# Optimization experiments

Measured on AMD Instinct MI355X. Metric: run time of the kernel, lower is better.

Reference implementation:

```python
import jax, jax.numpy as jnp
import numpy as np

B, F, C, H, W = 16, 256, 64, 64, 64   # batch, features, z_channels(e_dim), height, width
N_E = 512                              # codebooksize
BETA = 1.0
EPS = 1e-5


def setup_inputs() -> dict:
    key = jax.random.key(0)
    ks = jax.random.split(key, 4)
    x = jax.random.normal(ks[0], (B, F, H, W), jnp.float32)
    emb = jax.random.normal(ks[1], (N_E, C), jnp.float32)
    emb = emb / jnp.linalg.norm(emb, axis=1, keepdims=True)  # points on hypersphere
    return dict(
        x=x,
        bn1_gamma=jnp.ones((F,), jnp.float32),
        bn1_beta=jnp.zeros((F,), jnp.float32),
        conv1_w=jax.random.normal(ks[2], (C, F), jnp.float32) * np.float32(1.0 / np.sqrt(F)),
        conv1_b=jnp.zeros((C,), jnp.float32),
        conv2_w=jax.random.normal(ks[3], (C, C), jnp.float32) * np.float32(1.0 / np.sqrt(C)),
        conv2_b=jnp.zeros((C,), jnp.float32),
        embedding=emb,
        r=jnp.ones((N_E,), jnp.float32),
    )


def reference(x, bn1_gamma, bn1_beta, conv1_w, conv1_b, conv2_w, conv2_b, embedding, r):
    sg = jax.lax.stop_gradient
    # BatchNorm2d (training mode: batch stats, biased variance)
    mu = x.mean(axis=(0, 2, 3), keepdims=True)
    var = x.var(axis=(0, 2, 3), keepdims=True)
    x1 = (x - mu) * jax.lax.rsqrt(var + EPS)
    x1 = x1 * bn1_gamma[None, :, None, None] + bn1_beta[None, :, None, None]
    # 1x1 convs (note: original overwrites norm2 output, conv2 consumes conv1 output directly)
    x1 = jnp.einsum('bfhw,cf->bchw', x1, conv1_w) + conv1_b[None, :, None, None]
    z = jnp.einsum('bchw,oc->bohw', x1, conv2_w) + conv2_b[None, :, None, None]

    zf = z.reshape(-1, C)  # [B*C*H*W/e_dim view == flat rows of e_dim]
    # codebook angular statistics (norms detached, as torch.Tensor(list) detaches)
    d1 = embedding @ embedding.T                                 # [n_e, n_e]
    en = sg(jnp.linalg.norm(embedding, axis=1))                  # [n_e]
    edx = jnp.clip(d1 / (en[:, None] * en[None, :]), -0.99999, 0.99999)
    ang = jnp.arccos(edx)
    total_min_distance = jnp.mean(jnp.sort(ang, axis=0)[1])      # kthvalue(.,2,dim=0)
    codebookvariance = jnp.mean(jnp.var(ang, axis=1, ddof=1))    # torch.var unbiased

    # VQ dispatch: squared L2 distances + argmin + gather
    d = (zf ** 2).sum(1, keepdims=True) + (embedding ** 2).sum(1) - 2.0 * (zf @ embedding.T)
    idx = jnp.argmin(d, axis=1)                                  # [ntok]
    z_q = embedding[idx].reshape(z.shape)

    hsw = jnp.mean(jnp.square(r - en))
    # legacy=True path with beta=1.0, ignorezq=False, disentangle=True
    loss = jnp.mean((sg(z_q) - z) ** 2) + BETA * jnp.mean((z_q - sg(z)) ** 2)
    loss = loss + hsw + (codebookvariance - total_min_distance)

    z_q = z + sg(z_q - z)  # straight-through
    cb_loss = jnp.float32(0.0)  # prev_cb is None
    r_c = r + sg(jnp.clip(r, 0.9, 1.1) - r)  # Clamp with straight-through grad
    mean_r = jnp.mean(r_c)
    return (loss, z_q, codebookvariance, total_min_distance, hsw, cb_loss, mean_r)
```

## Files before the change

kernel.cpp:

```cpp
#include <hip/hip_runtime.h>
#include <math.h>


#define CAP    2048
#define MARGIN 4e-3f

#define WS_WHI  0
#define WS_WLO  8192
#define WS_BP   16384
#define WS_EN   16448
#define WS_E2   16960
#define WS_ACC  17472
#define WS_CNT  17480
#define WS_WL   17488
#define WS_EFT  19536
#define WS_WD   52304
#define WS_BPD  85072
#define WS_EHI  85200
#define WS_ELO  101584
#define WS_PART 117968

typedef __attribute__((ext_vector_type(8))) __bf16 bf16v8;
typedef __attribute__((ext_vector_type(2))) __bf16 bf16v2;
typedef __attribute__((ext_vector_type(4))) float  f32v4;
typedef __attribute__((ext_vector_type(4))) unsigned u32v4;

__device__ __forceinline__ unsigned short f2bf(float f) {
    __bf16 h = (__bf16)f;
    return __builtin_bit_cast(unsigned short, h);
}
__device__ __forceinline__ float bf2f(unsigned short h) {
    union { unsigned u; float f; } v; v.u = ((unsigned)h) << 16; return v.f;
}
__device__ __forceinline__ unsigned pack_bf2(float a, float b) {
    bf16v2 v = { (__bf16)a, (__bf16)b };
    return __builtin_bit_cast(unsigned, v);
}
__device__ __forceinline__ float bfhi(float a) {
    return (float)(__bf16)a;
}
__device__ __forceinline__ void load_lds16(const float* g, unsigned* l) {
    __builtin_amdgcn_global_load_lds((const __attribute__((address_space(1))) void*)g,
                                     (__attribute__((address_space(3))) void*)l, 16, 0, 0);
}

__global__ __launch_bounds__(256) void bn_partial(
    const float* __restrict__ x, double* __restrict__ part)
{
    const int t = threadIdx.x;
    const int f = blockIdx.x >> 2, ch = blockIdx.x & 3;
    double s0 = 0.0, s1 = 0.0, q0 = 0.0, q1 = 0.0, q2 = 0.0, q3 = 0.0;
    #pragma unroll
    for (int bb = 0; bb < 4; ++bb) {
        const int b = ch * 4 + bb;
        const float4* p = (const float4*)(x + ((size_t)(b * 256 + f) << 12));
        #pragma unroll
        for (int ii = 0; ii < 4; ++ii) {
            float4 u = p[t + ii * 256];
            double dx = u.x, dy = u.y, dz = u.z, dw = u.w;
            s0 += dx + dy; s1 += dz + dw;
            q0 = fma(dx, dx, q0); q1 = fma(dy, dy, q1);
            q2 = fma(dz, dz, q2); q3 = fma(dw, dw, q3);
        }
    }
    double s = s0 + s1, q = (q0 + q1) + (q2 + q3);
    #pragma unroll
    for (int off = 32; off; off >>= 1) { s += __shfl_xor(s, off, 64); q += __shfl_xor(q, off, 64); }
    __shared__ double sh[8];
    const int wv = t >> 6;
    if ((t & 63) == 0) { sh[wv * 2] = s; sh[wv * 2 + 1] = q; }
    __syncthreads();
    if (t == 0) {
        part[blockIdx.x * 2]     = (sh[0] + sh[2]) + (sh[4] + sh[6]);
        part[blockIdx.x * 2 + 1] = (sh[1] + sh[3]) + (sh[5] + sh[7]);
    }
}

__global__ __launch_bounds__(256) void prep(
    const float* __restrict__ w1, const float* __restrict__ w2,
    const float* __restrict__ b1, const float* __restrict__ b2,
    const float* __restrict__ gamma, const float* __restrict__ beta,
    const float* __restrict__ emb, const double* __restrict__ part,
    unsigned short* __restrict__ whi, unsigned short* __restrict__ wlo,
    double* __restrict__ Wd,
    double* __restrict__ bpd, float* __restrict__ bp,
    float* __restrict__ eft, float* __restrict__ en, float* __restrict__ e2,
    unsigned short* __restrict__ ehi, unsigned short* __restrict__ elo,
    float* __restrict__ accs, int* __restrict__ cnt)
{
    __shared__ double sh_ad[4];
    __shared__ double cdl[256];
    __shared__ double red[4][64];
    __shared__ double tsh[64];
    const int t = threadIdx.x;

    if (blockIdx.x < 64) {
        const int o = t & 63, fi = t >> 6;
        const int f = blockIdx.x * 4 + fi;
        if (o == 0) {
            double s = (part[(4 * f) * 2]     + part[(4 * f + 1) * 2])
                     + (part[(4 * f + 2) * 2] + part[(4 * f + 3) * 2]);
            double q = (part[(4 * f) * 2 + 1]     + part[(4 * f + 1) * 2 + 1])
                     + (part[(4 * f + 2) * 2 + 1] + part[(4 * f + 3) * 2 + 1]);
            double mean = s * (1.0 / 65536.0);
            double var  = q * (1.0 / 65536.0) - mean * mean;
            sh_ad[fi] = (double)gamma[f] / sqrt(var + 1e-5);
        }
        __syncthreads();
        double s = 0.0;
        for (int c = 0; c < 64; ++c)
            s = fma((double)w2[o * 64 + c], (double)w1[c * 256 + f], s);
        double wp = s * sh_ad[fi];
        Wd[o * 256 + f] = wp;
        {
            float wpf = (float)wp;
            unsigned short wh = f2bf(wpf);
            unsigned short wlv = f2bf(wpf - bf2f(wh));
            int mt = o >> 4, cq_ = o & 15, sK = f >> 5, qd_ = (f >> 3) & 3, j = f & 7;
            int idx = ((mt * 8 + sK) * 64 + qd_ * 16 + cq_) * 8 + j;
            whi[idx] = wh; wlo[idx] = wlv;
        }

        const int lane = t & 63, wv = t >> 6;
        #pragma unroll
        for (int rr = 0; rr < 2; ++rr) {
            int n = blockIdx.x * 8 + rr * 4 + wv;
            float v = emb[n * 64 + lane];
            eft[lane * 512 + n] = v;
            unsigned short hb = f2bf(v);
            unsigned short lb = f2bf(v - bf2f(hb));
            int pos = (lane >> 3) ^ (n & 7);
            ehi[n * 64 + pos * 8 + (lane & 7)] = hb;
            elo[n * 64 + pos * 8 + (lane & 7)] = lb;
            float qq = v * v;
            #pragma unroll
            for (int off = 32; off; off >>= 1) qq += __shfl_xor(qq, off, 64);
            if (lane == 0) { e2[n] = qq; en[n] = sqrtf(qq); }
        }
    } else {
        {
            const int f = t;
            double s = (part[(4 * f) * 2]     + part[(4 * f + 1) * 2])
                     + (part[(4 * f + 2) * 2] + part[(4 * f + 3) * 2]);
            double q = (part[(4 * f) * 2 + 1]     + part[(4 * f + 1) * 2 + 1])
                     + (part[(4 * f + 2) * 2 + 1] + part[(4 * f + 3) * 2 + 1]);
            double mean = s * (1.0 / 65536.0);
            double var  = q * (1.0 / 65536.0) - mean * mean;
            double a = (double)gamma[f] / sqrt(var + 1e-5);
            cdl[f] = (double)beta[f] - mean * a;
        }
        __syncthreads();
        const int o = t & 63, p = t >> 6;
        double ss = 0.0;
        for (int j = 0; j < 64; ++j) {
            int fidx = p * 64 + j;
            ss = fma((double)w1[o * 256 + fidx], cdl[fidx], ss);
        }
        red[p][o] = ss; __syncthreads();
        if (t < 64) tsh[t] = (double)b1[t] + (red[0][t] + red[1][t]) + (red[2][t] + red[3][t]);
        __syncthreads();
        if (t < 64) {
            double bb = (double)b2[t];
            for (int c = 0; c < 64; ++c)
                bb = fma((double)w2[t * 64 + c], tsh[c], bb);
            bpd[t] = bb;
            bp[t]  = (float)bb;
        }
        if (t < 8) accs[t] = 0.f;
        if (t == 0) cnt[0] = 0;
    }
}

__global__ __launch_bounds__(256, 2) void fused_gemm_vq(
    const float* __restrict__ x,
    const unsigned short* __restrict__ whi,
    const unsigned short* __restrict__ wlo,
    const float* __restrict__ bp,
    const float* __restrict__ emb,
    const float* __restrict__ e2,
    const float* __restrict__ en,
    const float* __restrict__ eft,
    const unsigned short* __restrict__ ehi,
    const unsigned short* __restrict__ elo,
    float* __restrict__ accs,
    int* __restrict__ cnt, int* __restrict__ wl,
    float* __restrict__ zq)
{
    __shared__ __align__(16) unsigned smem[4880];
    enum { OAR = 0,
           OE2 = 4096, OZ2 = 4608, ODT = 4672, OD2T = 4736, OIT = 4800 };
    float* e2s = (float*)(smem + OE2);
    float* z2s = (float*)(smem + OZ2);
    float* dT  = (float*)(smem + ODT);
    float* d2T = (float*)(smem + OD2T);
    int*   iT  = (int*)(smem + OIT);

    const int tid = threadIdx.x, lane = tid & 63, wv = tid >> 6;

    if (blockIdx.x >= 1024) {
        const int i = blockIdx.x - 1024;
        float* ang = e2s;
        const float eni = en[i];
        const float* ei = emb + (i << 6);
        #pragma unroll
        for (int jj = 0; jj < 2; ++jj) {
            const int j = tid + jj * 256;
            float d0 = 0.f, d1 = 0.f, d2 = 0.f, d3 = 0.f;
            #pragma unroll
            for (int k = 0; k < 64; k += 4) {
                d0 = fmaf(ei[k + 0], eft[(k + 0) * 512 + j], d0);
                d1 = fmaf(ei[k + 1], eft[(k + 1) * 512 + j], d1);
                d2 = fmaf(ei[k + 2], eft[(k + 2) * 512 + j], d2);
                d3 = fmaf(ei[k + 3], eft[(k + 3) * 512 + j], d3);
            }
            float dot = (d0 + d1) + (d2 + d3);
            float xv = dot / (eni * en[j]);
            xv = fminf(fmaxf(xv, -0.99999f), 0.99999f);
            ang[j] = acosf(xv);
        }
        __syncthreads();
        if (wv == 0) {
            float m1 = 3.4e38f, m2 = 3.4e38f, ssum = 0.f;
            #pragma unroll
            for (int t8 = 0; t8 < 8; ++t8) {
                float a = ang[t8 * 64 + lane];
                ssum += a;
                if (a < m1) { m2 = m1; m1 = a; }
                else if (a < m2) m2 = a;
            }
            #pragma unroll
            for (int off = 32; off; off >>= 1) ssum += __shfl_xor(ssum, off, 64);
            #pragma unroll
            for (int off = 32; off; off >>= 1) {
                float o1 = __shfl_xor(m1, off, 64);
                float o2 = __shfl_xor(m2, off, 64);
                if (o1 < m1) { m2 = fminf(m1, o2); m1 = o1; }
                else          m2 = fminf(m2, o1);
            }
            float mean = ssum * (1.f / 512.f);
            float vs = 0.f;
            #pragma unroll
            for (int t8 = 0; t8 < 8; ++t8) {
                float tt = ang[t8 * 64 + lane] - mean;
                vs = fmaf(tt, tt, vs);
            }
            #pragma unroll
            for (int off = 32; off; off >>= 1) vs += __shfl_xor(vs, off, 64);
            if (lane == 0) {
                atomicAdd(accs + 1, vs * (1.f / 511.f));
                atomicAdd(accs + 2, m2);
            }
        }
        return;
    }

    const int wvu = __builtin_amdgcn_readfirstlane(wv);
    const int b = blockIdx.x >> 6, h = blockIdx.x & 63;
    const int cq = lane & 15, qd = lane >> 4;

    bf16v8 Ahi[8], Alo[8];
    #pragma unroll
    for (int s = 0; s < 8; ++s) {
        Ahi[s] = *(const bf16v8*)(whi + ((size_t)((wvu * 8 + s) * 64 + lane)) * 8);
        Alo[s] = *(const bf16v8*)(wlo + ((size_t)((wvu * 8 + s) * 64 + lane)) * 8);
    }
    float bpv[4];
    #pragma unroll
    for (int r = 0; r < 4; ++r) bpv[r] = bp[wvu * 16 + qd * 4 + r];
    e2s[tid]       = e2[tid];
    e2s[tid + 256] = e2[tid + 256];

    const float* xb = x + ((size_t)(b * 256 + wvu * 16) << 12) + (h << 6) + lane;
    float xv[16];
    #pragma unroll
    for (int i = 0; i < 16; ++i) xv[i] = xb[(size_t)i << 12];

    f32v4 acc[4];
    #pragma unroll
    for (int nt = 0; nt < 4; ++nt) acc[nt] = (f32v4){bpv[0], bpv[1], bpv[2], bpv[3]};

    #pragma unroll
    for (int chk = 0; chk < 4; ++chk) {
        __syncthreads();
        {
            unsigned hb[8], lb[8];
            #pragma unroll
            for (int p = 0; p < 8; ++p) {
                float a = xv[2 * p], bq = xv[2 * p + 1];
                hb[p] = pack_bf2(a, bq);
                lb[p] = pack_bf2(a - bfhi(a), bq - bfhi(bq));
            }
            const int b0 = lane * 32 + (((2 * wvu) ^ (lane & 7)) << 2);
            const int b1 = lane * 32 + (((2 * wvu + 1) ^ (lane & 7)) << 2);
            *(u32v4*)(smem + OAR + b0)        = (u32v4){hb[0], hb[1], hb[2], hb[3]};
            *(u32v4*)(smem + OAR + b1)        = (u32v4){hb[4], hb[5], hb[6], hb[7]};
            *(u32v4*)(smem + OAR + 2048 + b0) = (u32v4){lb[0], lb[1], lb[2], lb[3]};
            *(u32v4*)(smem + OAR + 2048 + b1) = (u32v4){lb[4], lb[5], lb[6], lb[7]};
        }
        __syncthreads();
        if (chk < 3) {
            const float* xb2 = xb + ((size_t)((chk + 1) * 64) << 12);
            #pragma unroll
            for (int i = 0; i < 16; ++i) xv[i] = xb2[(size_t)i << 12];
        }
        #pragma unroll
        for (int st2 = 0; st2 < 2; ++st2) {
            const int s = chk * 2 + st2;
            #pragma unroll
            for (int nt = 0; nt < 4; ++nt) {
                const int row = nt * 16 + cq;
                const int pos = row * 32 + (((st2 * 4 + qd) ^ (row & 7)) << 2);
                bf16v8 bh = *(const bf16v8*)(smem + OAR + pos);
                bf16v8 bl = *(const bf16v8*)(smem + OAR + 2048 + pos);
                acc[nt] = __builtin_amdgcn_mfma_f32_16x16x32_bf16(Ahi[s], bh, acc[nt], 0, 0, 0);
                acc[nt] = __builtin_amdgcn_mfma_f32_16x16x32_bf16(Ahi[s], bl, acc[nt], 0, 0, 0);
                acc[nt] = __builtin_amdgcn_mfma_f32_16x16x32_bf16(Alo[s], bh, acc[nt], 0, 0, 0);
            }
        }
    }
    __syncthreads();

    {
        float z2p[4];
        #pragma unroll
        for (int r = 0; r < 4; ++r) {
            float p2 = 0.f;
            #pragma unroll
            for (int nt = 0; nt < 4; ++nt) p2 = fmaf(acc[nt][r], acc[nt][r], p2);
            #pragma unroll
            for (int off = 1; off <= 8; off <<= 1) p2 += __shfl_xor(p2, off, 64);
            z2p[r] = p2;
        }
        if (cq == 0) {
            #pragma unroll
            for (int r = 0; r < 4; ++r) z2s[wvu * 16 + qd * 4 + r] = z2p[r];
        }
        unsigned short* ar = (unsigned short*)(smem + OAR);
        #pragma unroll
        for (int nt = 0; nt < 4; ++nt) {
            const int w = nt * 16 + cq;
            const int gz = w >> 3, kj = w & 7;
            #pragma unroll
            for (int r = 0; r < 4; ++r) {
                const int tok = wvu * 16 + qd * 4 + r;
                const int hw = tok * 64 + ((gz ^ (tok & 7)) << 3) + kj;
                unsigned short zh = f2bf(acc[nt][r]);
                ar[hw]        = zh;
                ar[4096 + hw] = f2bf(acc[nt][r] - bf2f(zh));
            }
        }
    }
    __syncthreads();

    const int x7 = cq & 7;
    bf16v8 vahi[2], valo[2];
    {
        const int rbase = (wvu * 16 + cq) * 32;
        #pragma unroll
        for (int s = 0; s < 2; ++s) {
            int pos = ((s * 4 + qd) ^ x7) * 4;
            vahi[s] = *(const bf16v8*)(smem + OAR + rbase + pos);
            valo[s] = *(const bf16v8*)(smem + OAR + 2048 + rbase + pos);
        }
    }
    __syncthreads();

    {
        const float* gh = (const float*)ehi;
        const float* gl = (const float*)elo;
        load_lds16(gh + wvu * 256 + lane * 4,        smem + OAR + wvu * 256);
        load_lds16(gl + wvu * 256 + lane * 4,        smem + OAR + 1024 + wvu * 256);
        load_lds16(gh + 1024 + wvu * 256 + lane * 4, smem + OAR + 2048 + wvu * 256);
        load_lds16(gl + 1024 + wvu * 256 + lane * 4, smem + OAR + 3072 + wvu * 256);
    }

    float m1[4] = {-3.4e38f, -3.4e38f, -3.4e38f, -3.4e38f};
    float m2[4] = {-3.4e38f, -3.4e38f, -3.4e38f, -3.4e38f};
    int   i1[4] = {0, 0, 0, 0};
    const int p0 = (qd ^ x7) * 4, p1 = ((4 + qd) ^ x7) * 4;

    #pragma unroll 1
    for (int t2 = 0; t2 < 32; ++t2) {
        if ((t2 & 1) == 0) {
            __syncthreads();
            int st = t2 >> 1;
            if (st >= 1 && st < 15) {
                const float* gh = (const float*)ehi + (size_t)(st + 1) * 1024;
                const float* gl = (const float*)elo + (size_t)(st + 1) * 1024;
                unsigned* dst = smem + OAR + ((st + 1) & 1) * 2048;
                load_lds16(gh + wvu * 256 + lane * 4, dst + wvu * 256);
                load_lds16(gl + wvu * 256 + lane * 4, dst + 1024 + wvu * 256);
            }
        }
        const int rb = OAR + ((t2 >> 1) & 1) * 2048 + ((t2 & 1) * 16 + cq) * 32;
        bf16v8 bh0 = *(const bf16v8*)(smem + rb + p0);
        bf16v8 bh1 = *(const bf16v8*)(smem + rb + p1);
        bf16v8 bl0 = *(const bf16v8*)(smem + rb + 1024 + p0);
        bf16v8 bl1 = *(const bf16v8*)(smem + rb + 1024 + p1);
        const float eps = e2s[t2 * 16 + cq];
        f32v4 a = {0.f, 0.f, 0.f, 0.f};
        __builtin_amdgcn_s_setprio(1);
        a = __builtin_amdgcn_mfma_f32_16x16x32_bf16(vahi[0], bh0, a, 0, 0, 0);
        a = __builtin_amdgcn_mfma_f32_16x16x32_bf16(vahi[1], bh1, a, 0, 0, 0);
        a = __builtin_amdgcn_mfma_f32_16x16x32_bf16(vahi[0], bl0, a, 0, 0, 0);
        a = __builtin_amdgcn_mfma_f32_16x16x32_bf16(vahi[1], bl1, a, 0, 0, 0);
        a = __builtin_amdgcn_mfma_f32_16x16x32_bf16(valo[0], bh0, a, 0, 0, 0);
        a = __builtin_amdgcn_mfma_f32_16x16x32_bf16(valo[1], bh1, a, 0, 0, 0);
        __builtin_amdgcn_s_setprio(0);
        const int n = t2 * 16 + cq;
        #pragma unroll
        for (int r = 0; r < 4; ++r) {
            float s = fmaf(-0.5f, eps, a[r]);
            bool gt = s > m1[r];
            m2[r] = fminf(fmaxf(s, m2[r]), m1[r]);
            i1[r] = gt ? n : i1[r];
            m1[r] = fmaxf(s, m1[r]);
        }
    }

    #pragma unroll
    for (int r = 0; r < 4; ++r) {
        #pragma unroll
        for (int off = 1; off <= 8; off <<= 1) {
            float o1 = __shfl_xor(m1[r], off, 64);
            float o2 = __shfl_xor(m2[r], off, 64);
            int   oi = __shfl_xor(i1[r], off, 64);
            if (o1 > m1[r] || (o1 == m1[r] && oi < i1[r])) {
                m2[r] = fmaxf(m1[r], o2); m1[r] = o1; i1[r] = oi;
            } else {
                m2[r] = fmaxf(m2[r], o1);
            }
        }
    }
    if (cq == 0) {
        #pragma unroll
        for (int r = 0; r < 4; ++r) {
            int tok = wvu * 16 + qd * 4 + r;
            dT[tok] = m1[r]; d2T[tok] = m2[r]; iT[tok] = i1[r];
        }
    }
    __syncthreads();

    if (wv == 0) {
        float s1 = dT[lane], s2 = d2T[lane];
        if (s1 - s2 < MARGIN * 0.5f) {
            int pos = atomicAdd(cnt, 1);
            if (pos < CAP) wl[pos] = ((b << 6) + lane) * 64 + h;
        }
        float ms = z2s[lane] - 2.f * s1;
        #pragma unroll
        for (int off = 32; off; off >>= 1) ms += __shfl_xor(ms, off, 64);
        if (lane == 0) atomicAdd(accs + 0, ms);
    }
    __syncthreads();

    float* zrow = zq + ((size_t)(b * 64) << 12) + (h << 6) + lane;
    #pragma unroll
    for (int cc = 0; cc < 16; ++cc) {
        int c = wvu * 16 + cc;
        int id = iT[c];
        zrow[(size_t)c << 12] = emb[(id << 6) + lane];
    }
}

__global__ __launch_bounds__(256) void refine_fin(
    const float* __restrict__ x,
    const double* __restrict__ Wd,
    const double* __restrict__ bpd,
    const float* __restrict__ emb,
    const float* __restrict__ eft,
    const int* __restrict__ cnt, const int* __restrict__ wl,
    float* __restrict__ zq,
    const float* __restrict__ accs, const float* __restrict__ en,
    const float* __restrict__ r, float* __restrict__ out)
{
    const int tid = threadIdx.x, lane = tid & 63, wv = tid >> 6;

    if (blockIdx.x == 2048) {
        if (wv == 0) {
            float hs = 0.f, rs = 0.f;
            #pragma unroll
            for (int jj = 0; jj < 8; ++jj) {
                int n = (jj << 6) + lane;
                float rv = r[n];
                float d = rv - en[n];
                hs = fmaf(d, d, hs);
                rs += fminf(fmaxf(rv, 0.9f), 1.1f);
            }
            #pragma unroll
            for (int off = 32; off; off >>= 1) { hs += __shfl_xor(hs, off, 64); rs += __shfl_xor(rs, off, 64); }
            if (lane == 0) {
                float hsw    = hs * (1.f / 512.f);
                float mean_r = rs * (1.f / 512.f);
                float mse    = accs[0] * (1.f / 4194304.f);
                float cbv    = accs[1] * (1.f / 512.f);
                float tmd    = accs[2] * (1.f / 512.f);
                float loss   = 2.f * mse + hsw + (cbv - tmd);
                out[0]       = loss;
                out[4194305] = cbv;
                out[4194306] = tmd;
                out[4194307] = hsw;
                out[4194308] = 0.f;
                out[4194309] = mean_r;
            }
        }
        return;
    }

    int count = cnt[0]; if (count > CAP) count = CAP;
    const int it = blockIdx.x;
    if (it >= count) return;

    __shared__ double zp[4][64];
    __shared__ double zs[64];
    __shared__ double dsh[4];
    __shared__ int    ish[4];

    const int r2 = wl[it];
    const int b = r2 >> 12, c = (r2 >> 6) & 63, h = r2 & 63;

    {
        const float* xp = x + (((size_t)(b * 256 + wv * 64)) << 12) + (h << 6) + lane;
        const double* wrow = Wd + c * 256 + wv * 64;
        double zc0 = 0.0, zc1 = 0.0, zc2 = 0.0, zc3 = 0.0;
        double zc4 = 0.0, zc5 = 0.0, zc6 = 0.0, zc7 = 0.0;
        #pragma unroll
        for (int f = 0; f < 64; f += 8) {
            float a0 = xp[(size_t)(f + 0) << 12];
            float a1 = xp[(size_t)(f + 1) << 12];
            float a2 = xp[(size_t)(f + 2) << 12];
            float a3 = xp[(size_t)(f + 3) << 12];
            float a4 = xp[(size_t)(f + 4) << 12];
            float a5 = xp[(size_t)(f + 5) << 12];
            float a6 = xp[(size_t)(f + 6) << 12];
            float a7 = xp[(size_t)(f + 7) << 12];
            zc0 = fma(wrow[f + 0], (double)a0, zc0);
            zc1 = fma(wrow[f + 1], (double)a1, zc1);
            zc2 = fma(wrow[f + 2], (double)a2, zc2);
            zc3 = fma(wrow[f + 3], (double)a3, zc3);
            zc4 = fma(wrow[f + 4], (double)a4, zc4);
            zc5 = fma(wrow[f + 5], (double)a5, zc5);
            zc6 = fma(wrow[f + 6], (double)a6, zc6);
            zc7 = fma(wrow[f + 7], (double)a7, zc7);
        }
        zp[wv][lane] = ((zc0 + zc1) + (zc2 + zc3)) + ((zc4 + zc5) + (zc6 + zc7));
    }
    __syncthreads();
    if (tid < 64) zs[tid] = (zp[0][tid] + zp[1][tid]) + (zp[2][tid] + zp[3][tid]) + bpd[c];
    __syncthreads();

    const int n0 = tid, n1 = tid + 256;
    double d0a = 0.0, d0b = 0.0, d0c = 0.0, d0d = 0.0;
    double d1a = 0.0, d1b = 0.0, d1c = 0.0, d1d = 0.0;
    #pragma unroll 4
    for (int k = 0; k < 64; k += 4) {
        double z0 = zs[k], z1 = zs[k + 1], z2 = zs[k + 2], z3 = zs[k + 3];
        double t;
        t = z0 - (double)eft[((k + 0) << 9) + n0]; d0a = fma(t, t, d0a);
        t = z1 - (double)eft[((k + 1) << 9) + n0]; d0b = fma(t, t, d0b);
        t = z2 - (double)eft[((k + 2) << 9) + n0]; d0c = fma(t, t, d0c);
        t = z3 - (double)eft[((k + 3) << 9) + n0]; d0d = fma(t, t, d0d);
        t = z0 - (double)eft[((k + 0) << 9) + n1]; d1a = fma(t, t, d1a);
        t = z1 - (double)eft[((k + 1) << 9) + n1]; d1b = fma(t, t, d1b);
        t = z2 - (double)eft[((k + 2) << 9) + n1]; d1c = fma(t, t, d1c);
        t = z3 - (double)eft[((k + 3) << 9) + n1]; d1d = fma(t, t, d1d);
    }
    double d0 = (d0a + d0b) + (d0c + d0d);
    double d1 = (d1a + d1b) + (d1c + d1d);
    double dm; int im;
    if (d1 < d0) { dm = d1; im = n1; } else { dm = d0; im = n0; }

    #pragma unroll
    for (int off = 32; off; off >>= 1) {
        double od = __shfl_xor(dm, off, 64);
        int    oi = __shfl_xor(im, off, 64);
        if (od < dm || (od == dm && oi < im)) { dm = od; im = oi; }
    }
    if (lane == 0) { dsh[wv] = dm; ish[wv] = im; }
    __syncthreads();

    if (tid < 64) {
        double best = dsh[0]; int bi = ish[0];
        #pragma unroll
        for (int wq = 1; wq < 4; ++wq) {
            double od = dsh[wq]; int oi = ish[wq];
            if (od < best || (od == best && oi < bi)) { best = od; bi = oi; }
        }
        zq[((size_t)r2 << 6) + tid] = emb[(bi << 6) + tid];
    }
}

extern "C" void kernel_launch(void* const* d_in, const int* in_sizes, int n_in,
                              void* d_out, int out_size, void* d_ws, size_t ws_size,
                              hipStream_t stream) {
    const float* x   = (const float*)d_in[0];
    const float* g1  = (const float*)d_in[1];
    const float* be1 = (const float*)d_in[2];
    const float* w1  = (const float*)d_in[3];
    const float* b1  = (const float*)d_in[4];
    const float* w2  = (const float*)d_in[5];
    const float* b2  = (const float*)d_in[6];
    const float* emb = (const float*)d_in[7];
    const float* r   = (const float*)d_in[8];
    float* ws = (float*)d_ws;
    float* out = (float*)d_out;

    double* WD   = (double*)(ws + WS_WD);
    double* BPD  = (double*)(ws + WS_BPD);
    double* PART = (double*)(ws + WS_PART);
    int*    CNT  = (int*)(ws + WS_CNT);
    int*    WL   = (int*)(ws + WS_WL);
    unsigned short* WHI = (unsigned short*)(ws + WS_WHI);
    unsigned short* WLO = (unsigned short*)(ws + WS_WLO);
    unsigned short* EHI = (unsigned short*)(ws + WS_EHI);
    unsigned short* ELO = (unsigned short*)(ws + WS_ELO);

    bn_partial<<<1024, 256, 0, stream>>>(x, PART);
    prep<<<65, 256, 0, stream>>>(w1, w2, b1, b2, g1, be1, emb, PART,
                                 WHI, WLO, WD, BPD, ws + WS_BP,
                                 ws + WS_EFT, ws + WS_EN, ws + WS_E2,
                                 EHI, ELO, ws + WS_ACC, CNT);
    fused_gemm_vq<<<1536, 256, 0, stream>>>(x, WHI, WLO, ws + WS_BP,
                                            emb, ws + WS_E2, ws + WS_EN, ws + WS_EFT,
                                            EHI, ELO, ws + WS_ACC, CNT, WL, out + 1);
    refine_fin<<<2049, 256, 0, stream>>>(x, WD, BPD, emb, ws + WS_EFT, CNT, WL,
                                         out + 1, ws + WS_ACC, ws + WS_EN, r, out);
}
```

Baseline: 182.9 us.

## Move codebook angle stats and embedding prep into BN stats kernel; double-buffer x loads

The codebook angular statistics and embedding preprocessing move out of the GEMM/VQ and prep kernels into the first kernel, where they run alongside the BN partial reductions. Per-row variance and second-min values go to workspace arrays, which the final kernel reduces, replacing the float atomics. This shortens the critical path and lets the GEMM kernel launch only its 1024 real blocks. Inside the GEMM, x loads are double-buffered across two register sets so loads run two chunks ahead, at the cost of more registers.

```diff
diff --git a/kernel.cpp b/kernel.cpp
--- a/kernel.cpp
+++ b/kernel.cpp
@@ -19,6 +19,8 @@
 #define WS_EHI  85200
 #define WS_ELO  101584
 #define WS_PART 117968
+#define WS_SV   122064
+#define WS_SM   122576
 
 typedef __attribute__((ext_vector_type(8))) __bf16 bf16v8;
 typedef __attribute__((ext_vector_type(2))) __bf16 bf16v2;
@@ -44,35 +46,127 @@
                                      (__attribute__((address_space(3))) void*)l, 16, 0, 0);
 }
 
-__global__ __launch_bounds__(256) void bn_partial(
-    const float* __restrict__ x, double* __restrict__ part)
+__global__ __launch_bounds__(256) void bn_stats_prep(
+    const float* __restrict__ x, double* __restrict__ part,
+    const float* __restrict__ emb,
+    float* __restrict__ eft, float* __restrict__ en, float* __restrict__ e2,
+    unsigned short* __restrict__ ehi, unsigned short* __restrict__ elo,
+    float* __restrict__ sv, float* __restrict__ sm)
 {
     const int t = threadIdx.x;
-    const int f = blockIdx.x >> 2, ch = blockIdx.x & 3;
-    double s0 = 0.0, s1 = 0.0, q0 = 0.0, q1 = 0.0, q2 = 0.0, q3 = 0.0;
-    #pragma unroll
-    for (int bb = 0; bb < 4; ++bb) {
-        const int b = ch * 4 + bb;
-        const float4* p = (const float4*)(x + ((size_t)(b * 256 + f) << 12));
-        #pragma unroll
-        for (int ii = 0; ii < 4; ++ii) {
-            float4 u = p[t + ii * 256];
-            double dx = u.x, dy = u.y, dz = u.z, dw = u.w;
-            s0 += dx + dy; s1 += dz + dw;
-            q0 = fma(dx, dx, q0); q1 = fma(dy, dy, q1);
-            q2 = fma(dz, dz, q2); q3 = fma(dw, dw, q3);
-        }
-    }
-    double s = s0 + s1, q = (q0 + q1) + (q2 + q3);
-    #pragma unroll
-    for (int off = 32; off; off >>= 1) { s += __shfl_xor(s, off, 64); q += __shfl_xor(q, off, 64); }
-    __shared__ double sh[8];
-    const int wv = t >> 6;
-    if ((t & 63) == 0) { sh[wv * 2] = s; sh[wv * 2 + 1] = q; }
-    __syncthreads();
-    if (t == 0) {
-        part[blockIdx.x * 2]     = (sh[0] + sh[2]) + (sh[4] + sh[6]);
-        part[blockIdx.x * 2 + 1] = (sh[1] + sh[3]) + (sh[5] + sh[7]);
+
+    if (blockIdx.x < 1024) {
+        const int f = blockIdx.x >> 2, ch = blockIdx.x & 3;
+        double s0 = 0.0, s1 = 0.0, q0 = 0.0, q1 = 0.0, q2 = 0.0, q3 = 0.0;
+        #pragma unroll
+        for (int bb = 0; bb < 4; ++bb) {
+            const int b = ch * 4 + bb;
+            const float4* p = (const float4*)(x + ((size_t)(b * 256 + f) << 12));
+            #pragma unroll
+            for (int ii = 0; ii < 4; ++ii) {
+                float4 u = p[t + ii * 256];
+                double dx = u.x, dy = u.y, dz = u.z, dw = u.w;
+                s0 += dx + dy; s1 += dz + dw;
+                q0 = fma(dx, dx, q0); q1 = fma(dy, dy, q1);
+                q2 = fma(dz, dz, q2); q3 = fma(dw, dw, q3);
+            }
+        }
+        double s = s0 + s1, q = (q0 + q1) + (q2 + q3);
+        #pragma unroll
+        for (int off = 32; off; off >>= 1) { s += __shfl_xor(s, off, 64); q += __shfl_xor(q, off, 64); }
+        __shared__ double sh[8];
+        const int wv = t >> 6;
+        if ((t & 63) == 0) { sh[wv * 2] = s; sh[wv * 2 + 1] = q; }
+        __syncthreads();
+        if (t == 0) {
+            part[blockIdx.x * 2]     = (sh[0] + sh[2]) + (sh[4] + sh[6]);
+            part[blockIdx.x * 2 + 1] = (sh[1] + sh[3]) + (sh[5] + sh[7]);
+        }
+    } else if (blockIdx.x < 1088) {
+        const int blk = blockIdx.x - 1024;
+        const int lane = t & 63, wv = t >> 6;
+        #pragma unroll
+        for (int rr = 0; rr < 2; ++rr) {
+            int n = blk * 8 + rr * 4 + wv;
+            float v = emb[n * 64 + lane];
+            eft[lane * 512 + n] = v;
+            unsigned short hb = f2bf(v);
+            unsigned short lb = f2bf(v - bf2f(hb));
+            int pos = (lane >> 3) ^ (n & 7);
+            ehi[n * 64 + pos * 8 + (lane & 7)] = hb;
+            elo[n * 64 + pos * 8 + (lane & 7)] = lb;
+            float qq = v * v;
+            #pragma unroll
+            for (int off = 32; off; off >>= 1) qq += __shfl_xor(qq, off, 64);
+            if (lane == 0) { e2[n] = qq; en[n] = sqrtf(qq); }
+        }
+    } else {
+        const int i = blockIdx.x - 1088;
+        const int lane = t & 63, wv = t >> 6;
+        __shared__ float ei_sh[64];
+        __shared__ float ang[512];
+        if (t < 64) ei_sh[t] = emb[(i << 6) + t];
+        __syncthreads();
+        float ni0 = 0.f, ni1 = 0.f, ni2 = 0.f, ni3 = 0.f;
+        #pragma unroll
+        for (int k = 0; k < 64; k += 4) {
+            ni0 = fmaf(ei_sh[k + 0], ei_sh[k + 0], ni0);
+            ni1 = fmaf(ei_sh[k + 1], ei_sh[k + 1], ni1);
+            ni2 = fmaf(ei_sh[k + 2], ei_sh[k + 2], ni2);
+            ni3 = fmaf(ei_sh[k + 3], ei_sh[k + 3], ni3);
+        }
+        const float eni = sqrtf((ni0 + ni1) + (ni2 + ni3));
+        #pragma unroll
+        for (int jj = 0; jj < 2; ++jj) {
+            const int j = t + jj * 256;
+            const float4* er = (const float4*)(emb + ((size_t)j << 6));
+            float d0 = 0.f, d1 = 0.f, d2 = 0.f, d3 = 0.f;
+            float n0 = 0.f, n1 = 0.f, n2 = 0.f, n3 = 0.f;
+            #pragma unroll
+            for (int k4 = 0; k4 < 16; ++k4) {
+                float4 u = er[k4];
+                const float* e4 = ei_sh + k4 * 4;
+                d0 = fmaf(u.x, e4[0], d0); d1 = fmaf(u.y, e4[1], d1);
+                d2 = fmaf(u.z, e4[2], d2); d3 = fmaf(u.w, e4[3], d3);
+                n0 = fmaf(u.x, u.x, n0);   n1 = fmaf(u.y, u.y, n1);
+                n2 = fmaf(u.z, u.z, n2);   n3 = fmaf(u.w, u.w, n3);
+            }
+            float dot = (d0 + d1) + (d2 + d3);
+            float enj = sqrtf((n0 + n1) + (n2 + n3));
+            float xv = dot / (eni * enj);
+            xv = fminf(fmaxf(xv, -0.99999f), 0.99999f);
+            ang[j] = acosf(xv);
+        }
+        __syncthreads();
+        if (wv == 0) {
+            float m1 = 3.4e38f, m2 = 3.4e38f, ssum = 0.f;
+            #pragma unroll
+            for (int t8 = 0; t8 < 8; ++t8) {
+                float a = ang[t8 * 64 + lane];
+                ssum += a;
+                if (a < m1) { m2 = m1; m1 = a; }
+                else if (a < m2) m2 = a;
+            }
+            #pragma unroll
+            for (int off = 32; off; off >>= 1) ssum += __shfl_xor(ssum, off, 64);
+            #pragma unroll
+            for (int off = 32; off; off >>= 1) {
+                float o1 = __shfl_xor(m1, off, 64);
+                float o2 = __shfl_xor(m2, off, 64);
+                if (o1 < m1) { m2 = fminf(m1, o2); m1 = o1; }
+                else          m2 = fminf(m2, o1);
+            }
+            float mean = ssum * (1.f / 512.f);
+            float vs = 0.f;
+            #pragma unroll
+            for (int t8 = 0; t8 < 8; ++t8) {
+                float tt = ang[t8 * 64 + lane] - mean;
+                vs = fmaf(tt, tt, vs);
+            }
+            #pragma unroll
+            for (int off = 32; off; off >>= 1) vs += __shfl_xor(vs, off, 64);
+            if (lane == 0) { sv[i] = vs * (1.f / 511.f); sm[i] = m2; }
+        }
     }
 }
 
@@ -80,12 +174,10 @@
     const float* __restrict__ w1, const float* __restrict__ w2,
     const float* __restrict__ b1, const float* __restrict__ b2,
     const float* __restrict__ gamma, const float* __restrict__ beta,
-    const float* __restrict__ emb, const double* __restrict__ part,
+    const double* __restrict__ part,
     unsigned short* __restrict__ whi, unsigned short* __restrict__ wlo,
     double* __restrict__ Wd,
     double* __restrict__ bpd, float* __restrict__ bp,
-    float* __restrict__ eft, float* __restrict__ en, float* __restrict__ e2,
-    unsigned short* __restrict__ ehi, unsigned short* __restrict__ elo,
     float* __restrict__ accs, int* __restrict__ cnt)
 {
     __shared__ double sh_ad[4];
@@ -120,23 +212,6 @@
             int idx = ((mt * 8 + sK) * 64 + qd_ * 16 + cq_) * 8 + j;
             whi[idx] = wh; wlo[idx] = wlv;
         }
-
-        const int lane = t & 63, wv = t >> 6;
-        #pragma unroll
-        for (int rr = 0; rr < 2; ++rr) {
-            int n = blockIdx.x * 8 + rr * 4 + wv;
-            float v = emb[n * 64 + lane];
-            eft[lane * 512 + n] = v;
-            unsigned short hb = f2bf(v);
-            unsigned short lb = f2bf(v - bf2f(hb));
-            int pos = (lane >> 3) ^ (n & 7);
-            ehi[n * 64 + pos * 8 + (lane & 7)] = hb;
-            elo[n * 64 + pos * 8 + (lane & 7)] = lb;
-            float qq = v * v;
-            #pragma unroll
-            for (int off = 32; off; off >>= 1) qq += __shfl_xor(qq, off, 64);
-            if (lane == 0) { e2[n] = qq; en[n] = sqrtf(qq); }
-        }
     } else {
         {
             const int f = t;
@@ -178,8 +253,6 @@
     const float* __restrict__ bp,
     const float* __restrict__ emb,
     const float* __restrict__ e2,
-    const float* __restrict__ en,
-    const float* __restrict__ eft,
     const unsigned short* __restrict__ ehi,
     const unsigned short* __restrict__ elo,
     float* __restrict__ accs,
@@ -196,64 +269,6 @@
     int*   iT  = (int*)(smem + OIT);
 
     const int tid = threadIdx.x, lane = tid & 63, wv = tid >> 6;
-
-    if (blockIdx.x >= 1024) {
-        const int i = blockIdx.x - 1024;
-        float* ang = e2s;
-        const float eni = en[i];
-        const float* ei = emb + (i << 6);
-        #pragma unroll
-        for (int jj = 0; jj < 2; ++jj) {
-            const int j = tid + jj * 256;
-            float d0 = 0.f, d1 = 0.f, d2 = 0.f, d3 = 0.f;
-            #pragma unroll
-            for (int k = 0; k < 64; k += 4) {
-                d0 = fmaf(ei[k + 0], eft[(k + 0) * 512 + j], d0);
-                d1 = fmaf(ei[k + 1], eft[(k + 1) * 512 + j], d1);
-                d2 = fmaf(ei[k + 2], eft[(k + 2) * 512 + j], d2);
-                d3 = fmaf(ei[k + 3], eft[(k + 3) * 512 + j], d3);
-            }
-            float dot = (d0 + d1) + (d2 + d3);
-            float xv = dot / (eni * en[j]);
-            xv = fminf(fmaxf(xv, -0.99999f), 0.99999f);
-            ang[j] = acosf(xv);
-        }
-        __syncthreads();
-        if (wv == 0) {
-            float m1 = 3.4e38f, m2 = 3.4e38f, ssum = 0.f;
-            #pragma unroll
-            for (int t8 = 0; t8 < 8; ++t8) {
-                float a = ang[t8 * 64 + lane];
-                ssum += a;
-                if (a < m1) { m2 = m1; m1 = a; }
-                else if (a < m2) m2 = a;
-            }
-            #pragma unroll
-            for (int off = 32; off; off >>= 1) ssum += __shfl_xor(ssum, off, 64);
-            #pragma unroll
-            for (int off = 32; off; off >>= 1) {
-                float o1 = __shfl_xor(m1, off, 64);
-                float o2 = __shfl_xor(m2, off, 64);
-                if (o1 < m1) { m2 = fminf(m1, o2); m1 = o1; }
-                else          m2 = fminf(m2, o1);
-            }
-            float mean = ssum * (1.f / 512.f);
-            float vs = 0.f;
-            #pragma unroll
-            for (int t8 = 0; t8 < 8; ++t8) {
-                float tt = ang[t8 * 64 + lane] - mean;
-                vs = fmaf(tt, tt, vs);
-            }
-            #pragma unroll
-            for (int off = 32; off; off >>= 1) vs += __shfl_xor(vs, off, 64);
-            if (lane == 0) {
-                atomicAdd(accs + 1, vs * (1.f / 511.f));
-                atomicAdd(accs + 2, m2);
-            }
-        }
-        return;
-    }
-
     const int wvu = __builtin_amdgcn_readfirstlane(wv);
     const int b = blockIdx.x >> 6, h = blockIdx.x & 63;
     const int cq = lane & 15, qd = lane >> 4;
@@ -271,53 +286,62 @@
     e2s[tid + 256] = e2[tid + 256];
 
     const float* xb = x + ((size_t)(b * 256 + wvu * 16) << 12) + (h << 6) + lane;
-    float xv[16];
-    #pragma unroll
-    for (int i = 0; i < 16; ++i) xv[i] = xb[(size_t)i << 12];
+    float xva[16], xvb[16];
+    #pragma unroll
+    for (int i = 0; i < 16; ++i) xva[i] = xb[(size_t)i << 12];
+    #pragma unroll
+    for (int i = 0; i < 16; ++i) xvb[i] = xb[((size_t)(64 + i)) << 12];
 
     f32v4 acc[4];
     #pragma unroll
     for (int nt = 0; nt < 4; ++nt) acc[nt] = (f32v4){bpv[0], bpv[1], bpv[2], bpv[3]};
 
-    #pragma unroll
-    for (int chk = 0; chk < 4; ++chk) {
-        __syncthreads();
-        {
-            unsigned hb[8], lb[8];
-            #pragma unroll
-            for (int p = 0; p < 8; ++p) {
-                float a = xv[2 * p], bq = xv[2 * p + 1];
-                hb[p] = pack_bf2(a, bq);
-                lb[p] = pack_bf2(a - bfhi(a), bq - bfhi(bq));
-            }
-            const int b0 = lane * 32 + (((2 * wvu) ^ (lane & 7)) << 2);
-            const int b1 = lane * 32 + (((2 * wvu + 1) ^ (lane & 7)) << 2);
-            *(u32v4*)(smem + OAR + b0)        = (u32v4){hb[0], hb[1], hb[2], hb[3]};
-            *(u32v4*)(smem + OAR + b1)        = (u32v4){hb[4], hb[5], hb[6], hb[7]};
-            *(u32v4*)(smem + OAR + 2048 + b0) = (u32v4){lb[0], lb[1], lb[2], lb[3]};
-            *(u32v4*)(smem + OAR + 2048 + b1) = (u32v4){lb[4], lb[5], lb[6], lb[7]};
-        }
-        __syncthreads();
-        if (chk < 3) {
-            const float* xb2 = xb + ((size_t)((chk + 1) * 64) << 12);
-            #pragma unroll
-            for (int i = 0; i < 16; ++i) xv[i] = xb2[(size_t)i << 12];
-        }
-        #pragma unroll
-        for (int st2 = 0; st2 < 2; ++st2) {
-            const int s = chk * 2 + st2;
-            #pragma unroll
-            for (int nt = 0; nt < 4; ++nt) {
-                const int row = nt * 16 + cq;
-                const int pos = row * 32 + (((st2 * 4 + qd) ^ (row & 7)) << 2);
-                bf16v8 bh = *(const bf16v8*)(smem + OAR + pos);
-                bf16v8 bl = *(const bf16v8*)(smem + OAR + 2048 + pos);
-                acc[nt] = __builtin_amdgcn_mfma_f32_16x16x32_bf16(Ahi[s], bh, acc[nt], 0, 0, 0);
-                acc[nt] = __builtin_amdgcn_mfma_f32_16x16x32_bf16(Ahi[s], bl, acc[nt], 0, 0, 0);
-                acc[nt] = __builtin_amdgcn_mfma_f32_16x16x32_bf16(Alo[s], bh, acc[nt], 0, 0, 0);
-            }
-        }
-    }
+#define GEMM_CHUNK(CHK, CUR)                                                          \
+    {                                                                                 \
+        __syncthreads();                                                 \
+        {                                                                             \
+            unsigned hb[8], lb[8];                                                    \
+            _Pragma("unroll")                                                         \
+            for (int p = 0; p < 8; ++p) {                                             \
+                float a = CUR[2 * p], bq = CUR[2 * p + 1];                            \
+                hb[p] = pack_bf2(a, bq);                                              \
+                lb[p] = pack_bf2(a - bfhi(a), bq - bfhi(bq));                         \
+            }                                                                         \
+            const int b0 = lane * 32 + (((2 * wvu) ^ (lane & 7)) << 2);               \
+            const int b1 = lane * 32 + (((2 * wvu + 1) ^ (lane & 7)) << 2);           \
+            *(u32v4*)(smem + OAR + b0)        = (u32v4){hb[0], hb[1], hb[2], hb[3]};  \
+            *(u32v4*)(smem + OAR + b1)        = (u32v4){hb[4], hb[5], hb[6], hb[7]};  \
+            *(u32v4*)(smem + OAR + 2048 + b0) = (u32v4){lb[0], lb[1], lb[2], lb[3]};  \
+            *(u32v4*)(smem + OAR + 2048 + b1) = (u32v4){lb[4], lb[5], lb[6], lb[7]};  \
+        }                                                                             \
+        __syncthreads();                                                \
+        if (CHK < 2) {                               \
+            const float* xb2 = xb + ((size_t)((CHK + 2) * 64) << 12);                 \
+            _Pragma("unroll")                                                         \
+            for (int i = 0; i < 16; ++i) CUR[i] = xb2[(size_t)i << 12];               \
+        }                                                                             \
+        _Pragma("unroll")                                                             \
+        for (int st2 = 0; st2 < 2; ++st2) {                                           \
+            const int s = CHK * 2 + st2;                                              \
+            _Pragma("unroll")                                                         \
+            for (int nt = 0; nt < 4; ++nt) {                                          \
+                const int row = nt * 16 + cq;                                         \
+                const int pos = row * 32 + (((st2 * 4 + qd) ^ (row & 7)) << 2);       \
+                bf16v8 bh = *(const bf16v8*)(smem + OAR + pos);                       \
+                bf16v8 bl = *(const bf16v8*)(smem + OAR + 2048 + pos);                \
+                acc[nt] = __builtin_amdgcn_mfma_f32_16x16x32_bf16(Ahi[s], bh, acc[nt], 0, 0, 0); \
+                acc[nt] = __builtin_amdgcn_mfma_f32_16x16x32_bf16(Ahi[s], bl, acc[nt], 0, 0, 0); \
+                acc[nt] = __builtin_amdgcn_mfma_f32_16x16x32_bf16(Alo[s], bh, acc[nt], 0, 0, 0); \
+            }                                                                         \
+        }                                                                             \
+    }
+
+    GEMM_CHUNK(0, xva)
+    GEMM_CHUNK(1, xvb)
+    GEMM_CHUNK(2, xva)
+    GEMM_CHUNK(3, xvb)
+#undef GEMM_CHUNK
+
     __syncthreads();
 
     {
@@ -472,13 +496,14 @@
     const int* __restrict__ cnt, const int* __restrict__ wl,
     float* __restrict__ zq,
     const float* __restrict__ accs, const float* __restrict__ en,
+    const float* __restrict__ sv, const float* __restrict__ sm,
     const float* __restrict__ r, float* __restrict__ out)
 {
     const int tid = threadIdx.x, lane = tid & 63, wv = tid >> 6;
 
     if (blockIdx.x == 2048) {
         if (wv == 0) {
-            float hs = 0.f, rs = 0.f;
+            float hs = 0.f, rs = 0.f, cv = 0.f, tm = 0.f;
             #pragma unroll
             for (int jj = 0; jj < 8; ++jj) {
                 int n = (jj << 6) + lane;
@@ -486,15 +511,20 @@
                 float d = rv - en[n];
                 hs = fmaf(d, d, hs);
                 rs += fminf(fmaxf(rv, 0.9f), 1.1f);
-            }
-            #pragma unroll
-            for (int off = 32; off; off >>= 1) { hs += __shfl_xor(hs, off, 64); rs += __shfl_xor(rs, off, 64); }
+                cv += sv[n];
+                tm += sm[n];
+            }
+            #pragma unroll
+            for (int off = 32; off; off >>= 1) {
+                hs += __shfl_xor(hs, off, 64); rs += __shfl_xor(rs, off, 64);
+                cv += __shfl_xor(cv, off, 64); tm += __shfl_xor(tm, off, 64);
+            }
             if (lane == 0) {
                 float hsw    = hs * (1.f / 512.f);
                 float mean_r = rs * (1.f / 512.f);
                 float mse    = accs[0] * (1.f / 4194304.f);
-                float cbv    = accs[1] * (1.f / 512.f);
-                float tmd    = accs[2] * (1.f / 512.f);
+                float cbv    = cv * (1.f / 512.f);
+                float tmd    = tm * (1.f / 512.f);
                 float loss   = 2.f * mse + hsw + (cbv - tmd);
                 out[0]       = loss;
                 out[4194305] = cbv;
@@ -615,14 +645,16 @@
     unsigned short* EHI = (unsigned short*)(ws + WS_EHI);
     unsigned short* ELO = (unsigned short*)(ws + WS_ELO);
 
-    bn_partial<<<1024, 256, 0, stream>>>(x, PART);
-    prep<<<65, 256, 0, stream>>>(w1, w2, b1, b2, g1, be1, emb, PART,
+    bn_stats_prep<<<1600, 256, 0, stream>>>(x, PART, emb,
+                                            ws + WS_EFT, ws + WS_EN, ws + WS_E2,
+                                            EHI, ELO, ws + WS_SV, ws + WS_SM);
+    prep<<<65, 256, 0, stream>>>(w1, w2, b1, b2, g1, be1, PART,
                                  WHI, WLO, WD, BPD, ws + WS_BP,
-                                 ws + WS_EFT, ws + WS_EN, ws + WS_E2,
-                                 EHI, ELO, ws + WS_ACC, CNT);
-    fused_gemm_vq<<<1536, 256, 0, stream>>>(x, WHI, WLO, ws + WS_BP,
-                                            emb, ws + WS_E2, ws + WS_EN, ws + WS_EFT,
+                                 ws + WS_ACC, CNT);
+    fused_gemm_vq<<<1024, 256, 0, stream>>>(x, WHI, WLO, ws + WS_BP,
+                                            emb, ws + WS_E2,
                                             EHI, ELO, ws + WS_ACC, CNT, WL, out + 1);
     refine_fin<<<2049, 256, 0, stream>>>(x, WD, BPD, emb, ws + WS_EFT, CNT, WL,
-                                         out + 1, ws + WS_ACC, ws + WS_EN, r, out);
-}
+                                         out + 1, ws + WS_ACC, ws + WS_EN,
+                                         ws + WS_SV, ws + WS_SM, r, out);
+}
```

After: 183.8 us. About the same (+0.5%).
